# Kernel tuning notes

Measured on AMD Instinct MI355X. Metric: run time of the kernel, lower is better.

The kernel has to match this reference:

```python
import jax, jax.numpy as jnp
import numpy as np

T = 4096
D_MODEL = 1024
H = 16          # n_heads
HD = 64         # head_dim = d_model // n_heads
LW = 64         # local_window
LT = 16         # latent_tokens
CHUNK = 32      # remote_chunk_size


def setup_inputs() -> dict:
    key = jax.random.key(0)
    ks = jax.random.split(key, 11)
    s = 0.02
    return {
        "x":  jax.random.normal(ks[0], (T, D_MODEL), dtype=jnp.float32),
        "Wq": jax.random.normal(ks[1], (D_MODEL, D_MODEL), dtype=jnp.float32) * s,
        "bq": jnp.zeros((D_MODEL,), dtype=jnp.float32),
        "Wk": jax.random.normal(ks[2], (D_MODEL, D_MODEL), dtype=jnp.float32) * s,
        "bk": jnp.zeros((D_MODEL,), dtype=jnp.float32),
        "Wv": jax.random.normal(ks[3], (D_MODEL, D_MODEL), dtype=jnp.float32) * s,
        "bv": jnp.zeros((D_MODEL,), dtype=jnp.float32),
        "Wo": jax.random.normal(ks[4], (D_MODEL, D_MODEL), dtype=jnp.float32) * s,
        "bo": jnp.zeros((D_MODEL,), dtype=jnp.float32),
        "Wg": jax.random.normal(ks[5], (H, D_MODEL), dtype=jnp.float32) * s,
        "bg": jnp.zeros((H,), dtype=jnp.float32),
    }


def reference(x, Wq, bq, Wk, bk, Wv, bv, Wo, bo, Wg, bg):
    """Runs prefill: forward_step for each token, returning per-step outputs [T, D_MODEL].

    Local cache = circular FIFO of size LW (append + pop-oldest == ring overwrite;
    softmax is permutation-invariant so slot order is irrelevant).
    Evicted tokens accumulate in pending sums; every CHUNK evictions the mean k/v
    is written into the remote latent ring of size LT (oldest overwritten).
    Attention happens BEFORE appending the current token's k/v, matching the torch code.
    """
    scale = 1.0 / np.sqrt(HD)
    Tn = x.shape[0]
    Q = (x @ Wq.T + bq).reshape(Tn, H, HD)
    K = (x @ Wk.T + bk).reshape(Tn, H, HD)
    V = (x @ Wv.T + bv).reshape(Tn, H, HD)
    G = jax.nn.sigmoid(x @ Wg.T + bg)  # [T, H] simple gate

    z = lambda *s: jnp.zeros(s, dtype=x.dtype)
    init = (z(LW, H, HD), z(LW, H, HD),   # local k/v ring
            z(LT, H, HD), z(LT, H, HD),   # remote k/v ring
            z(H, HD), z(H, HD),           # pending k/v sums
            jnp.int32(0), jnp.int32(0))   # pending count, remote count

    def step(carry, inp):
        lk, lv, rk, rv, pks, pvs, pc, rc = carry
        q, k, v, g, t = inp
        # ---- local attention over filled slots (count = min(t, LW)) ----
        lvalid = jnp.arange(LW) < jnp.minimum(t, LW)
        ls = jnp.einsum('hd,nhd->hn', q, lk) * scale
        ls = jnp.where(lvalid[None, :], ls, -1e30)
        lo = jnp.einsum('hn,nhd->hd', jax.nn.softmax(ls, axis=-1), lv)
        lo = lo * (t > 0)
        # ---- remote (compressed latent) attention ----
        rvalid = jnp.arange(LT) < jnp.minimum(rc, LT)
        rs = jnp.einsum('hd,nhd->hn', q, rk) * scale
        rs = jnp.where(rvalid[None, :], rs, -1e30)
        ro = jnp.einsum('hn,nhd->hd', jax.nn.softmax(rs, axis=-1), rv)
        ro = ro * (rc > 0)
        # ---- gate and combine ----
        gate = g[:, None]
        out = gate * lo + (1.0 - gate) * ro  # [H, HD]
        # ---- append k/v: ring write evicts token t-LW into pending ----
        pos = jnp.mod(t, LW)
        evict = (t >= LW)
        pks = pks + jnp.where(evict, lk[pos], 0.0)
        pvs = pvs + jnp.where(evict, lv[pos], 0.0)
        pc = pc + evict.astype(jnp.int32)
        lk = lk.at[pos].set(k)
        lv = lv.at[pos].set(v)
        # ---- compress pending into remote ring when CHUNK reached ----
        comp = (pc == CHUNK)
        ridx = jnp.mod(rc, LT)
        rk = jnp.where(comp, rk.at[ridx].set(pks / CHUNK), rk)
        rv = jnp.where(comp, rv.at[ridx].set(pvs / CHUNK), rv)
        rc = rc + comp.astype(jnp.int32)
        pks = jnp.where(comp, 0.0, pks)
        pvs = jnp.where(comp, 0.0, pvs)
        pc = jnp.where(comp, 0, pc)
        return (lk, lv, rk, rv, pks, pvs, pc, rc), out

    ts = jnp.arange(Tn, dtype=jnp.int32)
    _, outs = jax.lax.scan(step, init, (Q, K, V, G, ts))
    return outs.reshape(Tn, D_MODEL) @ Wo.T + bo
```

## Files before the change

### kernel.cpp

```cpp
#include <hip/hip_runtime.h>
#include <hip/hip_bf16.h>
#include <math.h>

typedef __attribute__((ext_vector_type(8))) short short8;
typedef __attribute__((ext_vector_type(4))) float f32x4;

#define TT 4096
#define DM 1024
#define NH 16
#define HD 64
#define PSTR 168

typedef __attribute__((address_space(3))) unsigned int lds_u32;
typedef __attribute__((address_space(1))) unsigned int glb_u32;

__device__ __forceinline__ void async_cp16(const void* g, void* l) {
    __builtin_amdgcn_global_load_lds((glb_u32*)g, (lds_u32*)l, 16, 0, 0);
}

__device__ __forceinline__ float bf2f(unsigned short u) {
    union { unsigned int i; float f; } v;
    v.i = (unsigned int)u << 16;
    return v.f;
}

__global__ __launch_bounds__(256) void cast_all(
    const float* __restrict__ x,  const float* __restrict__ wq,
    const float* __restrict__ wk, const float* __restrict__ wv,
    const float* __restrict__ wo, const float* __restrict__ wg,
    __hip_bfloat16* __restrict__ xb,  __hip_bfloat16* __restrict__ wqb,
    __hip_bfloat16* __restrict__ wkb, __hip_bfloat16* __restrict__ wvb,
    __hip_bfloat16* __restrict__ wob, __hip_bfloat16* __restrict__ wgb)
{
    int b = blockIdx.x;
    const float* src;
    __hip_bfloat16* dst;
    size_t base;
    if (b < 4096)      { src = x;  dst = xb;  base = (size_t)b * 1024; }
    else if (b < 5120) { src = wq; dst = wqb; base = (size_t)(b - 4096) * 1024; }
    else if (b < 6144) { src = wk; dst = wkb; base = (size_t)(b - 5120) * 1024; }
    else if (b < 7168) { src = wv; dst = wvb; base = (size_t)(b - 6144) * 1024; }
    else if (b < 8192) { src = wo; dst = wob; base = (size_t)(b - 7168) * 1024; }
    else               { src = wg; dst = wgb; base = (size_t)(b - 8192) * 1024; }
    size_t i = base + (size_t)threadIdx.x * 4;
    float4 v = *(const float4*)(src + i);
    __hip_bfloat16 h0 = (__hip_bfloat16)v.x;
    __hip_bfloat16 h1 = (__hip_bfloat16)v.y;
    __hip_bfloat16 h2 = (__hip_bfloat16)v.z;
    __hip_bfloat16 h3 = (__hip_bfloat16)v.w;
    ushort4 u;
    u.x = *(unsigned short*)&h0;
    u.y = *(unsigned short*)&h1;
    u.z = *(unsigned short*)&h2;
    u.w = *(unsigned short*)&h3;
    *(ushort4*)((unsigned short*)dst + i) = u;
}

template <typename OutT>
__global__ __launch_bounds__(256) void gemm128(
    const __hip_bfloat16* __restrict__ A,
    const __hip_bfloat16* __restrict__ B0, const __hip_bfloat16* __restrict__ B1,
    const __hip_bfloat16* __restrict__ B2,
    const float* __restrict__ c0, const float* __restrict__ c1, const float* __restrict__ c2,
    OutT* __restrict__ O0, OutT* __restrict__ O1, OutT* __restrict__ O2)
{
    const int K = DM;
    __shared__ __align__(16) unsigned short sA[128 * 32];
    __shared__ __align__(16) unsigned short sB[128 * 32];

    const int grp = blockIdx.y >> 3;
    const __hip_bfloat16* B = grp == 0 ? B0 : (grp == 1 ? B1 : B2);
    const float* bias       = grp == 0 ? c0 : (grp == 1 ? c1 : c2);
    OutT* O                 = grp == 0 ? O0 : (grp == 1 ? O1 : O2);

    const int tid  = threadIdx.x;
    const int w    = tid >> 6;
    const int lane = tid & 63;
    const int l16  = lane & 15;
    const int quad = lane >> 4;
    const int rowBase = blockIdx.x * 128;
    const int colBase = (blockIdx.y & 7) * 128;

    const int srow   = lane >> 2;
    const int sswz   = (srow & 3) ^ (srow >> 2);
    const int gchunk = (lane & 3) ^ sswz;
    const __hip_bfloat16* gA = A + (size_t)(rowBase + w * 32 + srow) * K + gchunk * 8;
    const __hip_bfloat16* gB = B + (size_t)(colBase + w * 32 + srow) * K + gchunk * 8;
    unsigned short* lA = sA + w * 32 * 32;
    unsigned short* lB = sB + w * 32 * 32;

    const int fswz = (l16 & 3) ^ (l16 >> 2);
    const int mrow = (w & 1) * 64;
    const int ncol = (w >> 1) * 64;

    f32x4 acc[4][4];
#pragma unroll
    for (int i = 0; i < 4; ++i)
#pragma unroll
        for (int j = 0; j < 4; ++j) acc[i][j] = (f32x4){0.f, 0.f, 0.f, 0.f};

    for (int k0 = 0; k0 < K; k0 += 32) {
        __syncthreads();
        async_cp16(gA + k0, lA);
        async_cp16(gA + k0 + (size_t)16 * K, lA + 16 * 32);
        async_cp16(gB + k0, lB);
        async_cp16(gB + k0 + (size_t)16 * K, lB + 16 * 32);
        __syncthreads();

        short8 af[4], bf[4];
#pragma unroll
        for (int mt = 0; mt < 4; ++mt)
            af[mt] = *(const short8*)&sA[(mrow + mt * 16 + l16) * 32 + (quad ^ fswz) * 8];
#pragma unroll
        for (int nt = 0; nt < 4; ++nt)
            bf[nt] = *(const short8*)&sB[(ncol + nt * 16 + l16) * 32 + (quad ^ fswz) * 8];
#pragma unroll
        for (int mt = 0; mt < 4; ++mt)
#pragma unroll
            for (int nt = 0; nt < 4; ++nt)
                acc[mt][nt] = __builtin_amdgcn_mfma_f32_16x16x32_bf16(af[mt], bf[nt], acc[mt][nt], 0, 0, 0);
    }

#pragma unroll
    for (int nt = 0; nt < 4; ++nt) {
        int col = colBase + ncol + nt * 16 + l16;
        float bv = bias[col];
#pragma unroll
        for (int mt = 0; mt < 4; ++mt) {
#pragma unroll
            for (int r = 0; r < 4; ++r) {
                int row = rowBase + mrow + mt * 16 + quad * 4 + r;
                O[(size_t)row * DM + col] = (OutT)(acc[mt][nt][r] + bv);
            }
        }
    }
}

template <typename OutT>
__global__ __launch_bounds__(256) void gemm_n64(
    const __hip_bfloat16* __restrict__ A,
    const __hip_bfloat16* __restrict__ B,
    const float* __restrict__ bias,
    OutT* __restrict__ O)
{
    const int K = DM;
    __shared__ __align__(16) unsigned short sA[128 * 32];
    __shared__ __align__(16) unsigned short sB[64 * 32];

    const int tid  = threadIdx.x;
    const int w    = tid >> 6;
    const int lane = tid & 63;
    const int l16  = lane & 15;
    const int quad = lane >> 4;
    const int rowBase = blockIdx.x * 128;
    const int colBase = blockIdx.y * 64;

    const int srow   = lane >> 2;
    const int sswz   = (srow & 3) ^ (srow >> 2);
    const int gchunk = (lane & 3) ^ sswz;
    const __hip_bfloat16* gA = A + (size_t)(rowBase + w * 32 + srow) * K + gchunk * 8;
    const __hip_bfloat16* gB = B + (size_t)(colBase + w * 16 + srow) * K + gchunk * 8;
    unsigned short* lA = sA + w * 32 * 32;
    unsigned short* lB = sB + w * 16 * 32;

    const int fswz = (l16 & 3) ^ (l16 >> 2);
    const int mrow = w * 32;

    f32x4 acc[2][4];
#pragma unroll
    for (int i = 0; i < 2; ++i)
#pragma unroll
        for (int j = 0; j < 4; ++j) acc[i][j] = (f32x4){0.f, 0.f, 0.f, 0.f};

    for (int k0 = 0; k0 < K; k0 += 32) {
        __syncthreads();
        async_cp16(gA + k0, lA);
        async_cp16(gA + k0 + (size_t)16 * K, lA + 16 * 32);
        async_cp16(gB + k0, lB);
        __syncthreads();

        short8 af[2], bf[4];
#pragma unroll
        for (int mt = 0; mt < 2; ++mt)
            af[mt] = *(const short8*)&sA[(mrow + mt * 16 + l16) * 32 + (quad ^ fswz) * 8];
#pragma unroll
        for (int nt = 0; nt < 4; ++nt)
            bf[nt] = *(const short8*)&sB[(nt * 16 + l16) * 32 + (quad ^ fswz) * 8];
#pragma unroll
        for (int mt = 0; mt < 2; ++mt)
#pragma unroll
            for (int nt = 0; nt < 4; ++nt)
                acc[mt][nt] = __builtin_amdgcn_mfma_f32_16x16x32_bf16(af[mt], bf[nt], acc[mt][nt], 0, 0, 0);
    }

#pragma unroll
    for (int nt = 0; nt < 4; ++nt) {
        int col = colBase + nt * 16 + l16;
        float bv = bias[col];
#pragma unroll
        for (int mt = 0; mt < 2; ++mt) {
#pragma unroll
            for (int r = 0; r < 4; ++r) {
                int row = rowBase + mrow + mt * 16 + quad * 4 + r;
                O[(size_t)row * DM + col] = (OutT)(acc[mt][nt][r] + bv);
            }
        }
    }
}

__global__ __launch_bounds__(256) void aux_kernel(
    const __hip_bfloat16* __restrict__ K,
    const __hip_bfloat16* __restrict__ V,
    const __hip_bfloat16* __restrict__ xb,
    const __hip_bfloat16* __restrict__ Wgb,
    const float* __restrict__ bg,
    __hip_bfloat16* __restrict__ CK,
    __hip_bfloat16* __restrict__ CV,
    float* __restrict__ G)
{
    const int b = blockIdx.x;
    if (b < 256) {
        const int c  = b >> 1;
        const int d0 = (b & 1) * 512 + threadIdx.x * 2;
        const unsigned short* Ku = (const unsigned short*)K;
        const unsigned short* Vu = (const unsigned short*)V;
        float ak0 = 0.f, ak1 = 0.f, av0 = 0.f, av1 = 0.f;
#pragma unroll 8
        for (int i = 0; i < 32; ++i) {
            size_t off = (size_t)(c * 32 + i) * DM + d0;
            ushort2 kv = *(const ushort2*)(Ku + off);
            ushort2 vv = *(const ushort2*)(Vu + off);
            ak0 += bf2f(kv.x); ak1 += bf2f(kv.y);
            av0 += bf2f(vv.x); av1 += bf2f(vv.y);
        }
        __hip_bfloat16 k0 = (__hip_bfloat16)(ak0 * (1.f / 32.f));
        __hip_bfloat16 k1 = (__hip_bfloat16)(ak1 * (1.f / 32.f));
        __hip_bfloat16 v0 = (__hip_bfloat16)(av0 * (1.f / 32.f));
        __hip_bfloat16 v1 = (__hip_bfloat16)(av1 * (1.f / 32.f));
        ushort2 ko, vo;
        ko.x = *(unsigned short*)&k0; ko.y = *(unsigned short*)&k1;
        vo.x = *(unsigned short*)&v0; vo.y = *(unsigned short*)&v1;
        *(ushort2*)((unsigned short*)CK + (size_t)c * DM + d0) = ko;
        *(ushort2*)((unsigned short*)CV + (size_t)c * DM + d0) = vo;
        return;
    }
    const int unit = threadIdx.x >> 6;
    const int lane = threadIdx.x & 63;
    const int l16  = lane & 15;
    const int quad = lane >> 4;
    const int t0   = (b - 256) * 64 + unit * 16;
    const __hip_bfloat16* ap = xb  + (size_t)(t0 + l16) * DM + quad * 8;
    const __hip_bfloat16* bp = Wgb + (size_t)l16 * DM + quad * 8;
    f32x4 acc = (f32x4){0.f, 0.f, 0.f, 0.f};
#pragma unroll 4
    for (int k0 = 0; k0 < DM; k0 += 32) {
        short8 a = *(const short8*)(ap + k0);
        short8 bb = *(const short8*)(bp + k0);
        acc = __builtin_amdgcn_mfma_f32_16x16x32_bf16(a, bb, acc, 0, 0, 0);
    }
    float bgv = bg[l16];
#pragma unroll
    for (int r = 0; r < 4; ++r) {
        int t = t0 + quad * 4 + r;
        float z = acc[r] + bgv;
        G[t * NH + l16] = 1.f / (1.f + __expf(-z));
    }
}

__global__ __launch_bounds__(256) void attn_mfma(
    const __hip_bfloat16* __restrict__ Q,
    const __hip_bfloat16* __restrict__ K,
    const __hip_bfloat16* __restrict__ V,
    const __hip_bfloat16* __restrict__ CK,
    const __hip_bfloat16* __restrict__ CV,
    const float* __restrict__ G,
    __hip_bfloat16* __restrict__ Aout)
{
    __shared__ alignas(16) unsigned short Pls[64 * PSTR];
    __shared__ alignas(16) unsigned short Vts[64 * PSTR];

    const int h   = blockIdx.y;
    const int t0  = blockIdx.x * 64;
    const int tid = threadIdx.x;
    const int w    = tid >> 6;
    const int lane = tid & 63;
    const int l16  = lane & 15;
    const int quad = lane >> 4;
    const float scale = 0.125f;

    const int rc0  = (t0 >= 96) ? ((t0 - 64) >> 5) : 0;
    const int cmin = rc0 > 16 ? rc0 - 16 : 0;

    const unsigned short* Vu  = (const unsigned short*)V;
    const unsigned short* CVu = (const unsigned short*)CV;

    {
#pragma unroll
        for (int gg = 0; gg < 2; ++gg) {
            const int g = w * 2 + gg;
#pragma unroll
            for (int i = 0; i < 2; ++i) {
                const int pair = lane + 64 * i;
                if (pair < 80) {
                    const int j = pair * 2;
                    const unsigned short *s0, *s1;
                    if (j < 128) {
                        int tok0 = t0 - 64 + j; if (tok0 < 0) tok0 = 0;
                        int tok1 = t0 - 63 + j; if (tok1 < 0) tok1 = 0;
                        s0 = Vu + (size_t)tok0 * DM + h * 64 + g * 8;
                        s1 = Vu + (size_t)tok1 * DM + h * 64 + g * 8;
                    } else {
                        int c0 = cmin + (j - 128); if (c0 > 127) c0 = 127;
                        int c1 = c0 + 1;           if (c1 > 127) c1 = 127;
                        s0 = CVu + (size_t)c0 * DM + h * 64 + g * 8;
                        s1 = CVu + (size_t)c1 * DM + h * 64 + g * 8;
                    }
                    short8 v0 = *(const short8*)s0;
                    short8 v1 = *(const short8*)s1;
#pragma unroll
                    for (int e = 0; e < 8; ++e) {
                        ushort2 pk;
                        pk.x = (unsigned short)v0[e];
                        pk.y = (unsigned short)v1[e];
                        *(ushort2*)&Vts[(g * 8 + e) * PSTR + j] = pk;
                    }
                }
            }
        }
    }

    const __hip_bfloat16* qp = Q + (size_t)(t0 + w * 16 + l16) * DM + h * 64 + quad * 8;
    short8 qf0 = *(const short8*)(qp);
    short8 qf1 = *(const short8*)(qp + 32);

    f32x4 sc[8];
#pragma unroll
    for (int jt = 0; jt < 8; ++jt) {
        int j = jt * 16 + l16;
        int tok = t0 - 64 + j;
        tok = tok < 0 ? 0 : tok;
        const __hip_bfloat16* kp = K + (size_t)tok * DM + h * 64 + quad * 8;
        short8 b0 = *(const short8*)(kp);
        short8 b1 = *(const short8*)(kp + 32);
        f32x4 a = __builtin_amdgcn_mfma_f32_16x16x32_bf16(qf0, b0, (f32x4){0.f,0.f,0.f,0.f}, 0, 0, 0);
        sc[jt]  = __builtin_amdgcn_mfma_f32_16x16x32_bf16(qf1, b1, a, 0, 0, 0);
    }
    f32x4 sc2[2];
#pragma unroll
    for (int jt = 0; jt < 2; ++jt) {
        int c = cmin + jt * 16 + l16;
        if (c > 127) c = 127;
        const __hip_bfloat16* cp = CK + (size_t)c * DM + h * 64 + quad * 8;
        short8 b0 = *(const short8*)(cp);
        short8 b1 = *(const short8*)(cp + 32);
        f32x4 a = __builtin_amdgcn_mfma_f32_16x16x32_bf16(qf0, b0, (f32x4){0.f,0.f,0.f,0.f}, 0, 0, 0);
        sc2[jt] = __builtin_amdgcn_mfma_f32_16x16x32_bf16(qf1, b1, a, 0, 0, 0);
    }

    __syncthreads();

    const int rbase = w * 16 + quad * 4;
    float gl[4], g2[4];
    float mx[4], sm[4], mx2[4], sm2[4];
#pragma unroll
    for (int reg = 0; reg < 4; ++reg) {
        int rr = rbase + reg;
        int t  = t0 + rr;
        float g = G[t * NH + h];
        int rc = (t >= 96) ? ((t - 64) >> 5) : 0;
        gl[reg] = (t > 0)  ? g        : 0.f;
        g2[reg] = (rc > 0) ? (1.f - g) : 0.f;

        int jlo = rr > (64 - t0) ? rr : (64 - t0);
        int jhi = rr + 63;
        float m = -1e30f;
#pragma unroll
        for (int jt = 0; jt < 8; ++jt) {
            int j = jt * 16 + l16;
            float s = (j >= jlo && j <= jhi) ? sc[jt][reg] * scale : -1e30f;
            sc[jt][reg] = s;
            m = fmaxf(m, s);
        }
        mx[reg] = m;

        int nvis = rc < 16 ? rc : 16;
        int clo = rc - nvis, chi = rc - 1;
        float m2 = -1e30f;
#pragma unroll
        for (int jt = 0; jt < 2; ++jt) {
            int c = cmin + jt * 16 + l16;
            float s = (c >= clo && c <= chi) ? sc2[jt][reg] * scale : -1e30f;
            sc2[jt][reg] = s;
            m2 = fmaxf(m2, s);
        }
        mx2[reg] = m2;
    }
#pragma unroll
    for (int off = 1; off <= 8; off <<= 1)
#pragma unroll
        for (int reg = 0; reg < 4; ++reg) {
            mx[reg]  = fmaxf(mx[reg],  __shfl_xor(mx[reg],  off));
            mx2[reg] = fmaxf(mx2[reg], __shfl_xor(mx2[reg], off));
        }
#pragma unroll
    for (int reg = 0; reg < 4; ++reg) {
        float s = 0.f, s2 = 0.f;
#pragma unroll
        for (int jt = 0; jt < 8; ++jt) {
            float p = __expf(sc[jt][reg] - mx[reg]);
            sc[jt][reg] = p;
            s += p;
        }
#pragma unroll
        for (int jt = 0; jt < 2; ++jt) {
            float p = __expf(sc2[jt][reg] - mx2[reg]);
            sc2[jt][reg] = p;
            s2 += p;
        }
        sm[reg] = s; sm2[reg] = s2;
    }
#pragma unroll
    for (int off = 1; off <= 8; off <<= 1)
#pragma unroll
        for (int reg = 0; reg < 4; ++reg) {
            sm[reg]  += __shfl_xor(sm[reg],  off);
            sm2[reg] += __shfl_xor(sm2[reg], off);
        }

#pragma unroll
    for (int reg = 0; reg < 4; ++reg) {
        float f1 = gl[reg] / sm[reg];
        float f2 = g2[reg] / sm2[reg];
        int rowoff = (rbase + reg) * PSTR;
#pragma unroll
        for (int jt = 0; jt < 8; ++jt) {
            __hip_bfloat16 hb = (__hip_bfloat16)(sc[jt][reg] * f1);
            Pls[rowoff + jt * 16 + l16] = *(unsigned short*)&hb;
        }
#pragma unroll
        for (int jt = 0; jt < 2; ++jt) {
            __hip_bfloat16 hb = (__hip_bfloat16)(sc2[jt][reg] * f2);
            Pls[rowoff + 128 + jt * 16 + l16] = *(unsigned short*)&hb;
        }
    }
    asm volatile("s_waitcnt lgkmcnt(0)" ::: "memory");

    f32x4 o[4];
#pragma unroll
    for (int nt = 0; nt < 4; ++nt) o[nt] = (f32x4){0.f, 0.f, 0.f, 0.f};
#pragma unroll
    for (int kt = 0; kt < 5; ++kt) {
        short8 a = *(const short8*)&Pls[(w * 16 + l16) * PSTR + kt * 32 + quad * 8];
#pragma unroll
        for (int nt = 0; nt < 4; ++nt) {
            int dd = nt * 16 + l16;
            short8 b = *(const short8*)&Vts[dd * PSTR + kt * 32 + quad * 8];
            o[nt] = __builtin_amdgcn_mfma_f32_16x16x32_bf16(a, b, o[nt], 0, 0, 0);
        }
    }

#pragma unroll
    for (int nt = 0; nt < 4; ++nt) {
#pragma unroll
        for (int reg = 0; reg < 4; ++reg) {
            int row = t0 + rbase + reg;
            int col = h * 64 + nt * 16 + l16;
            Aout[(size_t)row * DM + col] = (__hip_bfloat16)(o[nt][reg]);
        }
    }
}

extern "C" void kernel_launch(void* const* d_in, const int* in_sizes, int n_in,
                              void* d_out, int out_size, void* d_ws, size_t ws_size,
                              hipStream_t stream)
{
    const float* x  = (const float*)d_in[0];
    const float* Wq = (const float*)d_in[1];
    const float* bq = (const float*)d_in[2];
    const float* Wk = (const float*)d_in[3];
    const float* bk = (const float*)d_in[4];
    const float* Wv = (const float*)d_in[5];
    const float* bv = (const float*)d_in[6];
    const float* Wo = (const float*)d_in[7];
    const float* bo = (const float*)d_in[8];
    const float* Wg = (const float*)d_in[9];
    const float* bg = (const float*)d_in[10];
    float* out = (float*)d_out;

    char* ws = (char*)d_ws;
    const size_t MB = 1024 * 1024;
    __hip_bfloat16* xb  = (__hip_bfloat16*)(ws + 0 * MB);
    __hip_bfloat16* Qb  = (__hip_bfloat16*)(ws + 8 * MB);
    __hip_bfloat16* Kb  = (__hip_bfloat16*)(ws + 16 * MB);
    __hip_bfloat16* Vb  = (__hip_bfloat16*)(ws + 24 * MB);
    __hip_bfloat16* Ab  = (__hip_bfloat16*)(ws + 32 * MB);
    __hip_bfloat16* Wqb = (__hip_bfloat16*)(ws + 40 * MB);
    __hip_bfloat16* Wkb = (__hip_bfloat16*)(ws + 42 * MB);
    __hip_bfloat16* Wvb = (__hip_bfloat16*)(ws + 44 * MB);
    __hip_bfloat16* Wob = (__hip_bfloat16*)(ws + 46 * MB);
    __hip_bfloat16* CKb = (__hip_bfloat16*)(ws + 48 * MB);
    __hip_bfloat16* CVb = (__hip_bfloat16*)(ws + 48 * MB + 256*1024);
    float* Gf           = (float*)(ws + 48 * MB + 512 * 1024);
    __hip_bfloat16* Wgb = (__hip_bfloat16*)(ws + 48 * MB + 768*1024);

    cast_all<<<dim3(8208), 256, 0, stream>>>(x, Wq, Wk, Wv, Wo, Wg,
                                             xb, Wqb, Wkb, Wvb, Wob, Wgb);

    gemm128<__hip_bfloat16><<<dim3(32, 24), 256, 0, stream>>>(
        xb, Wqb, Wkb, Wvb, bq, bk, bv, Qb, Kb, Vb);
    aux_kernel<<<dim3(320), 256, 0, stream>>>(Kb, Vb, xb, Wgb, bg, CKb, CVb, Gf);
    attn_mfma<<<dim3(64, 16), 256, 0, stream>>>(Qb, Kb, Vb, CKb, CVb, Gf, Ab);
    gemm_n64<float><<<dim3(32, 16), 256, 0, stream>>>(Ab, Wob, bo, out);
}
```

Before: 178.3 us.

## Double-buffer LDS tiles in GEMM kernels with async prefetch two stages ahead

Both GEMM kernels now keep two LDS buffers per operand and issue global-to-LDS async copies for tile t+2 while MFMAs run on tile t, using explicit vmcnt waits and barriers in place of the two __syncthreads per iteration. This aims to hide global load latency behind compute in the QKV and output projections. It doubles shared memory per block, which may lower occupancy, and it depends on the hand-written waitcnt counts being correct.

```diff
diff --git a/kernel.cpp b/kernel.cpp
--- a/kernel.cpp
+++ b/kernel.cpp
@@ -65,8 +65,9 @@
     OutT* __restrict__ O0, OutT* __restrict__ O1, OutT* __restrict__ O2)
 {
     const int K = DM;
-    __shared__ __align__(16) unsigned short sA[128 * 32];
-    __shared__ __align__(16) unsigned short sB[128 * 32];
+    const int NT = 32;
+    __shared__ __align__(16) unsigned short sA[2 * 128 * 32];
+    __shared__ __align__(16) unsigned short sB[2 * 128 * 32];
 
     const int grp = blockIdx.y >> 3;
     const __hip_bfloat16* B = grp == 0 ? B0 : (grp == 1 ? B1 : B2);
@@ -86,8 +87,8 @@
     const int gchunk = (lane & 3) ^ sswz;
     const __hip_bfloat16* gA = A + (size_t)(rowBase + w * 32 + srow) * K + gchunk * 8;
     const __hip_bfloat16* gB = B + (size_t)(colBase + w * 32 + srow) * K + gchunk * 8;
-    unsigned short* lA = sA + w * 32 * 32;
-    unsigned short* lB = sB + w * 32 * 32;
+    unsigned short* lA0 = sA + w * 32 * 32;
+    unsigned short* lB0 = sB + w * 32 * 32;
 
     const int fswz = (l16 & 3) ^ (l16 >> 2);
     const int mrow = (w & 1) * 64;
@@ -99,21 +100,43 @@
 #pragma unroll
         for (int j = 0; j < 4; ++j) acc[i][j] = (f32x4){0.f, 0.f, 0.f, 0.f};
 
-    for (int k0 = 0; k0 < K; k0 += 32) {
-        __syncthreads();
-        async_cp16(gA + k0, lA);
-        async_cp16(gA + k0 + (size_t)16 * K, lA + 16 * 32);
-        async_cp16(gB + k0, lB);
-        async_cp16(gB + k0 + (size_t)16 * K, lB + 16 * 32);
-        __syncthreads();
-
+    async_cp16(gA,                     lA0);
+    async_cp16(gA + (size_t)16 * K,    lA0 + 16 * 32);
+    async_cp16(gB,                     lB0);
+    async_cp16(gB + (size_t)16 * K,    lB0 + 16 * 32);
+    async_cp16(gA + 32,                  lA0 + 128 * 32);
+    async_cp16(gA + 32 + (size_t)16 * K, lA0 + 128 * 32 + 16 * 32);
+    async_cp16(gB + 32,                  lB0 + 128 * 32);
+    async_cp16(gB + 32 + (size_t)16 * K, lB0 + 128 * 32 + 16 * 32);
+
+    for (int t = 0; t < NT; ++t) {
+        if (t == NT - 1) asm volatile("s_waitcnt vmcnt(0)" ::: "memory");
+        else             asm volatile("s_waitcnt vmcnt(4)" ::: "memory");
+        __builtin_amdgcn_s_barrier();
+
+        const unsigned short* pA = sA + (t & 1) * (128 * 32);
+        const unsigned short* pB = sB + (t & 1) * (128 * 32);
         short8 af[4], bf[4];
 #pragma unroll
         for (int mt = 0; mt < 4; ++mt)
-            af[mt] = *(const short8*)&sA[(mrow + mt * 16 + l16) * 32 + (quad ^ fswz) * 8];
+            af[mt] = *(const short8*)&pA[(mrow + mt * 16 + l16) * 32 + (quad ^ fswz) * 8];
 #pragma unroll
         for (int nt = 0; nt < 4; ++nt)
-            bf[nt] = *(const short8*)&sB[(ncol + nt * 16 + l16) * 32 + (quad ^ fswz) * 8];
+            bf[nt] = *(const short8*)&pB[(ncol + nt * 16 + l16) * 32 + (quad ^ fswz) * 8];
+        asm volatile("s_waitcnt lgkmcnt(0)" ::: "memory");
+        __builtin_amdgcn_sched_barrier(0);
+        __builtin_amdgcn_s_barrier();
+
+        if (t + 2 < NT) {
+            const int k2 = (t + 2) * 32;
+            unsigned short* dA = lA0 + (t & 1) * (128 * 32);
+            unsigned short* dB = lB0 + (t & 1) * (128 * 32);
+            async_cp16(gA + k2,                  dA);
+            async_cp16(gA + k2 + (size_t)16 * K, dA + 16 * 32);
+            async_cp16(gB + k2,                  dB);
+            async_cp16(gB + k2 + (size_t)16 * K, dB + 16 * 32);
+        }
+
 #pragma unroll
         for (int mt = 0; mt < 4; ++mt)
 #pragma unroll
@@ -144,8 +167,9 @@
     OutT* __restrict__ O)
 {
     const int K = DM;
-    __shared__ __align__(16) unsigned short sA[128 * 32];
-    __shared__ __align__(16) unsigned short sB[64 * 32];
+    const int NT = 32;
+    __shared__ __align__(16) unsigned short sA[2 * 128 * 32];
+    __shared__ __align__(16) unsigned short sB[2 * 64 * 32];
 
     const int tid  = threadIdx.x;
     const int w    = tid >> 6;
@@ -160,8 +184,8 @@
     const int gchunk = (lane & 3) ^ sswz;
     const __hip_bfloat16* gA = A + (size_t)(rowBase + w * 32 + srow) * K + gchunk * 8;
     const __hip_bfloat16* gB = B + (size_t)(colBase + w * 16 + srow) * K + gchunk * 8;
-    unsigned short* lA = sA + w * 32 * 32;
-    unsigned short* lB = sB + w * 16 * 32;
+    unsigned short* lA0 = sA + w * 32 * 32;
+    unsigned short* lB0 = sB + w * 16 * 32;
 
     const int fswz = (l16 & 3) ^ (l16 >> 2);
     const int mrow = w * 32;
@@ -172,20 +196,40 @@
 #pragma unroll
         for (int j = 0; j < 4; ++j) acc[i][j] = (f32x4){0.f, 0.f, 0.f, 0.f};
 
-    for (int k0 = 0; k0 < K; k0 += 32) {
-        __syncthreads();
-        async_cp16(gA + k0, lA);
-        async_cp16(gA + k0 + (size_t)16 * K, lA + 16 * 32);
-        async_cp16(gB + k0, lB);
-        __syncthreads();
-
+    async_cp16(gA,                  lA0);
+    async_cp16(gA + (size_t)16 * K, lA0 + 16 * 32);
+    async_cp16(gB,                  lB0);
+    async_cp16(gA + 32,                  lA0 + 128 * 32);
+    async_cp16(gA + 32 + (size_t)16 * K, lA0 + 128 * 32 + 16 * 32);
+    async_cp16(gB + 32,                  lB0 + 64 * 32);
+
+    for (int t = 0; t < NT; ++t) {
+        if (t == NT - 1) asm volatile("s_waitcnt vmcnt(0)" ::: "memory");
+        else             asm volatile("s_waitcnt vmcnt(3)" ::: "memory");
+        __builtin_amdgcn_s_barrier();
+
+        const unsigned short* pA = sA + (t & 1) * (128 * 32);
+        const unsigned short* pB = sB + (t & 1) * (64 * 32);
         short8 af[2], bf[4];
 #pragma unroll
         for (int mt = 0; mt < 2; ++mt)
-            af[mt] = *(const short8*)&sA[(mrow + mt * 16 + l16) * 32 + (quad ^ fswz) * 8];
+            af[mt] = *(const short8*)&pA[(mrow + mt * 16 + l16) * 32 + (quad ^ fswz) * 8];
 #pragma unroll
         for (int nt = 0; nt < 4; ++nt)
-            bf[nt] = *(const short8*)&sB[(nt * 16 + l16) * 32 + (quad ^ fswz) * 8];
+            bf[nt] = *(const short8*)&pB[(nt * 16 + l16) * 32 + (quad ^ fswz) * 8];
+        asm volatile("s_waitcnt lgkmcnt(0)" ::: "memory");
+        __builtin_amdgcn_sched_barrier(0);
+        __builtin_amdgcn_s_barrier();
+
+        if (t + 2 < NT) {
+            const int k2 = (t + 2) * 32;
+            unsigned short* dA = lA0 + (t & 1) * (128 * 32);
+            unsigned short* dB = lB0 + (t & 1) * (64 * 32);
+            async_cp16(gA + k2,                  dA);
+            async_cp16(gA + k2 + (size_t)16 * K, dA + 16 * 32);
+            async_cp16(gB + k2,                  dB);
+        }
+
 #pragma unroll
         for (int mt = 0; mt < 2; ++mt)
 #pragma unroll
```

Result: no change. 177.4 us (-0.5%).
